# Kernel tuning notes

Measured on AMD Instinct MI355X. Metric: run time of the kernel, lower is better.

Reference implementation:

```python
import jax, jax.numpy as jnp
import numpy as np

ORDER = 4          # signature truncation depth
SCALAR_TERM = True # leading 1 term, as in signatory.signature(..., scalar_term=True)
BATCH, STREAM, CHAN = 2048, 128, 5  # channel = path_dim + 1 (time + 4-dim path)


def _exp_levels(dx, m):
    """Tensor exponential of a single increment dx: levels dx^{(x)k}/k!, k=1..m.
    dx: (B, d). Returns list of (B, d**k) arrays."""
    levels = [dx]
    for k in range(2, m + 1):
        prev = levels[-1]  # (B, d**(k-1))
        levels.append((prev[:, :, None] * dx[:, None, :]).reshape(dx.shape[0], -1) / k)
    return levels


def _chen(S, E):
    """Chen's identity: (S tensor-multiply E) truncated to depth m.
    S, E: tuples/lists of (B, d**k) level arrays (level k at list index k-1)."""
    m = len(E)
    B = E[0].shape[0]
    out = []
    for k in range(m):  # output level k+1
        term = S[k] + E[k]
        for i in range(k):  # S level (i+1) tensor E level (k-i)
            a, b = S[i], E[k - 1 - i]
            term = term + (a[:, :, None] * b[:, None, :]).reshape(B, -1)
        out.append(term)
    return tuple(out)


def _signature(path, m, scalar_term):
    """Truncated path signature, flattened levels 1..m (optionally with leading 1).
    path: (B, T, d) -> (B, [1+] d + d^2 + ... + d^m)."""
    B, T, d = path.shape
    dx = jnp.moveaxis(path[:, 1:] - path[:, :-1], 1, 0)  # (T-1, B, d)
    init = tuple(jnp.zeros((B, d ** k), path.dtype) for k in range(1, m + 1))

    def step(S, inc):
        return _chen(S, _exp_levels(inc, m)), None

    S, _ = jax.lax.scan(step, init, dx)
    sig = jnp.concatenate(S, axis=1)
    if scalar_term:
        sig = jnp.concatenate([jnp.ones((B, 1), path.dtype), sig], axis=1)
    return sig


def setup_inputs() -> dict:
    key = jax.random.key(0)
    kx, ky = jax.random.split(key)
    x = jax.random.normal(kx, (BATCH, STREAM, CHAN), dtype=jnp.float32)
    y = jax.random.normal(ky, (BATCH, STREAM, CHAN), dtype=jnp.float32)
    sigma = jnp.ones((CHAN - 1,), dtype=jnp.float32)  # adversarial scaling params
    return {"x": x, "y": y, "sigma": sigma}


def reference(x, y, sigma):
    # adversarial scaling applied to x's non-time channels only (as in forward())
    mu = jnp.concatenate([x[..., :1], x[..., 1:] * sigma], axis=-1)
    nu = y
    # signatures computed once each and shared across kxx, kxy, kyy (same math)
    sx = _signature(mu, ORDER, SCALAR_TERM)  # (B, P)
    sy = _signature(nu, ORDER, SCALAR_TERM)  # (B, P)
    kxx = jnp.einsum('ip,jp->ij', sx, sx)
    kxy = jnp.einsum('ip,jp->ij', sx, sy)
    kyy = jnp.einsum('ip,jp->ij', sy, sy)
    return jnp.mean(kxx) - 2.0 * jnp.mean(kxy) + jnp.mean(kyy)
```

## Files before the change

### kernel.cpp

```cpp
#include <hip/hip_runtime.h>

typedef float v2f __attribute__((ext_vector_type(2)));

#define BATCH  2048
#define TLEN   128
#define CH     5
#define SIGDIM 780
#define PPB    4
#define NBLK   ((2 * BATCH) / PPB)
#define SEGR   64
#define RBLK   64
#define POISON 0xAAAAAAAAu

__global__ __launch_bounds__(256, 4) void sig_kernel(
    const float* __restrict__ x, const float* __restrict__ y,
    const float* __restrict__ sigma, float* __restrict__ part) {
  const int tid  = threadIdx.x;
  const int wave = tid >> 6;
  const int lane = tid & 63;
  const int h    = lane >> 5;
  const int u    = lane & 31;
  const bool isX = (blockIdx.x < NBLK / 2);
  const int pbase = (isX ? blockIdx.x : blockIdx.x - NBLK / 2) * PPB;
  const int path  = pbase + wave;
  const float* src = (isX ? x : y) + (size_t)path * (TLEN * CH) + h * (SEGR * CH);

  __shared__ __align__(16) float buf[2 * PPB][784];
  __shared__ float blockAcc[SIGDIM];

  for (int i = tid; i < SIGDIM; i += 256) blockAcc[i] = 0.f;

  const float sg0 = sigma[0], sg1 = sigma[1], sg2 = sigma[2], sg3 = sigma[3];

  float* bw = buf[wave * 2 + h];
  if (h == 1 && u < 8) bw[63 * 8 + u] = 0.f;
  const int lim = h ? 63 * CH : 64 * CH;
  for (int i = u; i < lim; i += 32) {
    int t = i / CH, c = i - CH * t;
    float v = src[i + CH] - src[i];
    if (isX && c > 0) {
      const float s = (c == 1) ? sg0 : (c == 2) ? sg1 : (c == 3) ? sg2 : sg3;
      v *= s;
    }
    bw[t * 8 + c] = v;
  }
  __syncthreads();

  const int  uc = u < 25 ? u : 24;
  const int  a_ = uc / 5, b_ = uc - 5 * a_;
  const bool act = (u < 25);

  float s1a = 0.f, s2 = 0.f;
  v2f   s3p0 = {0.f, 0.f}, s3p1 = {0.f, 0.f};
  float s3e = 0.f;
  v2f   s4p0[5] = {{0,0},{0,0},{0,0},{0,0},{0,0}};
  v2f   s4p1[5] = {{0,0},{0,0},{0,0},{0,0},{0,0}};
  float s4e[5]  = {0,0,0,0,0};

  const float* pa_ = bw + a_;
  const float* pb_ = bw + b_;

  for (int g = 0; g < 8; ++g) {
    const float* rg = bw + g * 64;
    const float* ra = pa_ + g * 64;
    const float* rb = pb_ + g * 64;
    #pragma unroll
    for (int k = 0; k < 8; ++k) {
      const float4 m = *(const float4*)(rg + k * 8);
      const float d0 = m.x, d1 = m.y, d2 = m.z, d3 = m.w;
      const float d4 = rg[k * 8 + 4];
      const float da = ra[k * 8];
      const float db = rb[k * 8];
      const float pa = s1a * (1.f / 6.f) + da * (1.f / 24.f);
      const float qa = s1a * 0.5f        + da * (1.f / 6.f);
      const float rr = s1a               + da * 0.5f;
      s1a += da;
      const float p2 = 0.5f * s2 + db * pa;
      const float q2 =        s2 + db * qa;
      s2 += db * rr;
      const v2f dc01 = {d0, d1};
      const v2f dc23 = {d2, d3};
      const v2f p2v  = {p2, p2};
      const v2f q2v  = {q2, q2};
      const v2f p30  = __builtin_elementwise_fma(dc01, p2v, s3p0);
      const v2f p31  = __builtin_elementwise_fma(dc23, p2v, s3p1);
      const float p3e = s3e + d4 * p2;
      s3p0 = __builtin_elementwise_fma(dc01, q2v, s3p0);
      s3p1 = __builtin_elementwise_fma(dc23, q2v, s3p1);
      s3e += d4 * q2;
      #pragma unroll
      for (int d = 0; d < 5; ++d) {
        const float dd = (d == 0) ? d0 : (d == 1) ? d1 : (d == 2) ? d2 : (d == 3) ? d3 : d4;
        const v2f ddv = {dd, dd};
        s4p0[d] = __builtin_elementwise_fma(ddv, p30, s4p0[d]);
        s4p1[d] = __builtin_elementwise_fma(ddv, p31, s4p1[d]);
        s4e[d] += dd * p3e;
      }
    }
  }

  float S3[5] = {s3p0.x, s3p0.y, s3p1.x, s3p1.y, s3e};
  float S4[5][5];
  #pragma unroll
  for (int d = 0; d < 5; ++d) {
    S4[0][d] = s4p0[d].x; S4[1][d] = s4p0[d].y;
    S4[2][d] = s4p1[d].x; S4[3][d] = s4p1[d].y;
    S4[4][d] = s4e[d];
  }

  if (h == 1 && act) {
    float* sgb = bw;
    if (b_ == 0) sgb[a_] = s1a;
    sgb[5 + uc] = s2;
    #pragma unroll
    for (int c = 0; c < 5; ++c) {
      sgb[30 + uc * 5 + c] = S3[c];
      #pragma unroll
      for (int d = 0; d < 5; ++d) sgb[155 + (uc * 5 + c) * 5 + d] = S4[c][d];
    }
  }
  __syncthreads();

  if (h == 0 && act) {
    const float* R = buf[wave * 2 + 1];
    const float o1 = s1a + R[a_];
    const float o2 = s2 + s1a * R[b_] + R[5 + uc];
    if (b_ == 0) atomicAdd(&blockAcc[a_], o1);
    atomicAdd(&blockAcc[5 + uc], o2);
    #pragma unroll
    for (int c = 0; c < 5; ++c) {
      const float o3 = S3[c] + s2 * R[c] + s1a * R[5 + b_ * 5 + c] + R[30 + uc * 5 + c];
      atomicAdd(&blockAcc[30 + uc * 5 + c], o3);
      #pragma unroll
      for (int d = 0; d < 5; ++d) {
        const float o4 = S4[c][d] + S3[c] * R[d] + s2 * R[5 + c * 5 + d]
                       + s1a * R[30 + (b_ * 5 + c) * 5 + d]
                       + R[155 + (uc * 5 + c) * 5 + d];
        atomicAdd(&blockAcc[155 + (uc * 5 + c) * 5 + d], o4);
      }
    }
  }
  __syncthreads();

  const float w = isX ? 1.0f : -1.0f;
  float* pp = part + (size_t)blockIdx.x * SIGDIM;
  for (int i = tid; i < SIGDIM; i += 256) pp[i] = w * blockAcc[i];
}

__global__ __launch_bounds__(256) void red_kernel(
    const float* __restrict__ part, float* __restrict__ acc2,
    unsigned int* __restrict__ counter, float* __restrict__ out) {
  const int tid = threadIdx.x;
  float4 s = {0.f, 0.f, 0.f, 0.f};
  if (tid < SIGDIM / 4) {
    const float* base = part + (size_t)blockIdx.x * (NBLK / RBLK) * SIGDIM + 4 * tid;
    #pragma unroll
    for (int r = 0; r < NBLK / RBLK; ++r) {
      const float4 v = *(const float4*)(base + (size_t)r * SIGDIM);
      s.x += v.x; s.y += v.y; s.z += v.z; s.w += v.w;
    }
    atomicAdd(&acc2[4 * tid + 0], s.x);
    atomicAdd(&acc2[4 * tid + 1], s.y);
    atomicAdd(&acc2[4 * tid + 2], s.z);
    atomicAdd(&acc2[4 * tid + 3], s.w);
  }

  __shared__ float red[4];
  __shared__ unsigned int lastFlag;
  __syncthreads();
  if (tid == 0) {
    __threadfence();
    unsigned int old = __hip_atomic_fetch_add(counter, 1u, __ATOMIC_ACQ_REL,
                                              __HIP_MEMORY_SCOPE_AGENT);
    lastFlag = (old == POISON + (RBLK - 1)) ? 1u : 0u;
  }
  __syncthreads();
  if (lastFlag) {
    float local = 0.f;
    if (tid < SIGDIM / 4) {
      float vx = __hip_atomic_load(&acc2[4 * tid + 0], __ATOMIC_RELAXED, __HIP_MEMORY_SCOPE_AGENT);
      float vy = __hip_atomic_load(&acc2[4 * tid + 1], __ATOMIC_RELAXED, __HIP_MEMORY_SCOPE_AGENT);
      float vz = __hip_atomic_load(&acc2[4 * tid + 2], __ATOMIC_RELAXED, __HIP_MEMORY_SCOPE_AGENT);
      float vw = __hip_atomic_load(&acc2[4 * tid + 3], __ATOMIC_RELAXED, __HIP_MEMORY_SCOPE_AGENT);
      local = vx * vx + vy * vy + vz * vz + vw * vw;
    }
    #pragma unroll
    for (int off = 32; off > 0; off >>= 1) local += __shfl_down(local, off, 64);
    if ((tid & 63) == 0) red[tid >> 6] = local;
    __syncthreads();
    if (tid == 0)
      out[0] = (red[0] + red[1] + red[2] + red[3]) / (2048.0f * 2048.0f);
  }
}

extern "C" void kernel_launch(void* const* d_in, const int* in_sizes, int n_in,
                              void* d_out, int out_size, void* d_ws, size_t ws_size,
                              hipStream_t stream) {
  const float* x     = (const float*)d_in[0];
  const float* y     = (const float*)d_in[1];
  const float* sigma = (const float*)d_in[2];
  float* out = (float*)d_out;
  float* part = (float*)d_ws;
  float* acc2 = (float*)((char*)d_ws + (size_t)NBLK * SIGDIM * sizeof(float));
  unsigned int* counter =
      (unsigned int*)((char*)d_ws + (size_t)NBLK * SIGDIM * sizeof(float)
                      + SIGDIM * sizeof(float));

  sig_kernel<<<dim3(NBLK), dim3(256), 0, stream>>>(x, y, sigma, part);
  red_kernel<<<dim3(RBLK), dim3(256), 0, stream>>>(part, acc2, counter, out);
}
```

Measured before the change: 103.3 us.

## Split each path into four segments and combine with two-level Chen merge

New measurement: 160.4 us. 1.55x slower.

```diff
diff --git a/kernel.cpp b/kernel.cpp
--- a/kernel.cpp
+++ b/kernel.cpp
@@ -6,13 +6,15 @@
 #define TLEN   128
 #define CH     5
 #define SIGDIM 780
-#define PPB    4
-#define NBLK   ((2 * BATCH) / PPB)
-#define SEGR   64
+#define NBLK   2048
+#define NPATH  4096
+#define SEGR   32
+#define SROW   264
 #define RBLK   64
+#define ROWSPB (NPATH / RBLK)
 #define POISON 0xAAAAAAAAu
 
-__global__ __launch_bounds__(256, 4) void sig_kernel(
+__global__ __launch_bounds__(256, 6) void sig_kernel(
     const float* __restrict__ x, const float* __restrict__ y,
     const float* __restrict__ sigma, float* __restrict__ part) {
   const int tid  = threadIdx.x;
@@ -20,21 +22,22 @@
   const int lane = tid & 63;
   const int h    = lane >> 5;
   const int u    = lane & 31;
+  const int q    = wave & 1;
+  const int lp   = wave >> 1;
   const bool isX = (blockIdx.x < NBLK / 2);
-  const int pbase = (isX ? blockIdx.x : blockIdx.x - NBLK / 2) * PPB;
-  const int path  = pbase + wave;
-  const float* src = (isX ? x : y) + (size_t)path * (TLEN * CH) + h * (SEGR * CH);
-
-  __shared__ __align__(16) float buf[2 * PPB][784];
-  __shared__ float blockAcc[SIGDIM];
-
-  for (int i = tid; i < SIGDIM; i += 256) blockAcc[i] = 0.f;
+  const int pbase = (isX ? blockIdx.x : blockIdx.x - NBLK / 2) * 2;
+  const int path  = pbase + lp;
+  const int segIdx = 2 * q + h;
+  const float* src = (isX ? x : y) + (size_t)path * (TLEN * CH) + segIdx * (SEGR * CH);
+
+  __shared__ __align__(16) float segbuf[8][SROW];
+  __shared__ float sigbuf[4][SIGDIM];
 
   const float sg0 = sigma[0], sg1 = sigma[1], sg2 = sigma[2], sg3 = sigma[3];
 
-  float* bw = buf[wave * 2 + h];
-  if (h == 1 && u < 8) bw[63 * 8 + u] = 0.f;
-  const int lim = h ? 63 * CH : 64 * CH;
+  float* bw = segbuf[wave * 2 + h];
+  if (segIdx == 3 && u < 8) bw[31 * 8 + u] = 0.f;
+  const int lim = (segIdx == 3) ? 31 * CH : 32 * CH;
   for (int i = u; i < lim; i += 32) {
     int t = i / CH, c = i - CH * t;
     float v = src[i + CH] - src[i];
@@ -60,7 +63,7 @@
   const float* pa_ = bw + a_;
   const float* pb_ = bw + b_;
 
-  for (int g = 0; g < 8; ++g) {
+  for (int g = 0; g < 4; ++g) {
     const float* rg = bw + g * 64;
     const float* ra = pa_ + g * 64;
     const float* rb = pb_ + g * 64;
@@ -109,7 +112,7 @@
   }
 
   if (h == 1 && act) {
-    float* sgb = bw;
+    float* sgb = sigbuf[wave];
     if (b_ == 0) sgb[a_] = s1a;
     sgb[5 + uc] = s2;
     #pragma unroll
@@ -121,41 +124,77 @@
   }
   __syncthreads();
 
+  float o1 = 0.f, o2 = 0.f, o3[5], o4[5][5];
   if (h == 0 && act) {
-    const float* R = buf[wave * 2 + 1];
-    const float o1 = s1a + R[a_];
-    const float o2 = s2 + s1a * R[b_] + R[5 + uc];
-    if (b_ == 0) atomicAdd(&blockAcc[a_], o1);
-    atomicAdd(&blockAcc[5 + uc], o2);
-    #pragma unroll
-    for (int c = 0; c < 5; ++c) {
-      const float o3 = S3[c] + s2 * R[c] + s1a * R[5 + b_ * 5 + c] + R[30 + uc * 5 + c];
-      atomicAdd(&blockAcc[30 + uc * 5 + c], o3);
-      #pragma unroll
-      for (int d = 0; d < 5; ++d) {
-        const float o4 = S4[c][d] + S3[c] * R[d] + s2 * R[5 + c * 5 + d]
-                       + s1a * R[30 + (b_ * 5 + c) * 5 + d]
-                       + R[155 + (uc * 5 + c) * 5 + d];
-        atomicAdd(&blockAcc[155 + (uc * 5 + c) * 5 + d], o4);
-      }
+    const float* R = sigbuf[wave];
+    o1 = s1a + R[a_];
+    o2 = s2 + s1a * R[b_] + R[5 + uc];
+    #pragma unroll
+    for (int c = 0; c < 5; ++c) {
+      o3[c] = S3[c] + s2 * R[c] + s1a * R[5 + b_ * 5 + c] + R[30 + uc * 5 + c];
+      #pragma unroll
+      for (int d = 0; d < 5; ++d)
+        o4[c][d] = S4[c][d] + S3[c] * R[d] + s2 * R[5 + c * 5 + d]
+                 + s1a * R[30 + (b_ * 5 + c) * 5 + d]
+                 + R[155 + (uc * 5 + c) * 5 + d];
+    }
+  }
+  if (q == 1 && h == 0 && act) {
+    float* sgb = sigbuf[wave];
+    if (b_ == 0) sgb[a_] = o1;
+    sgb[5 + uc] = o2;
+    #pragma unroll
+    for (int c = 0; c < 5; ++c) {
+      sgb[30 + uc * 5 + c] = o3[c];
+      #pragma unroll
+      for (int d = 0; d < 5; ++d) sgb[155 + (uc * 5 + c) * 5 + d] = o4[c][d];
+    }
+  }
+  __syncthreads();
+
+  if (q == 0 && h == 0 && act) {
+    const float* R = sigbuf[wave + 1];
+    float f1 = o1 + R[a_];
+    float f2 = o2 + o1 * R[b_] + R[5 + uc];
+    float f3[5], f4[5][5];
+    #pragma unroll
+    for (int c = 0; c < 5; ++c) {
+      f3[c] = o3[c] + o2 * R[c] + o1 * R[5 + b_ * 5 + c] + R[30 + uc * 5 + c];
+      #pragma unroll
+      for (int d = 0; d < 5; ++d)
+        f4[c][d] = o4[c][d] + o3[c] * R[d] + o2 * R[5 + c * 5 + d]
+                 + o1 * R[30 + (b_ * 5 + c) * 5 + d]
+                 + R[155 + (uc * 5 + c) * 5 + d];
+    }
+    float* sgb = sigbuf[wave];
+    if (b_ == 0) sgb[a_] = f1;
+    sgb[5 + uc] = f2;
+    #pragma unroll
+    for (int c = 0; c < 5; ++c) {
+      sgb[30 + uc * 5 + c] = f3[c];
+      #pragma unroll
+      for (int d = 0; d < 5; ++d) sgb[155 + (uc * 5 + c) * 5 + d] = f4[c][d];
     }
   }
   __syncthreads();
 
   const float w = isX ? 1.0f : -1.0f;
-  float* pp = part + (size_t)blockIdx.x * SIGDIM;
-  for (int i = tid; i < SIGDIM; i += 256) pp[i] = w * blockAcc[i];
+  for (int i = tid; i < 2 * SIGDIM; i += 256) {
+    const int p = (i < SIGDIM) ? 0 : 1;
+    const int j = i - p * SIGDIM;
+    part[(size_t)(blockIdx.x * 2 + p) * SIGDIM + j] = w * sigbuf[2 * p][j];
+  }
 }
 
 __global__ __launch_bounds__(256) void red_kernel(
     const float* __restrict__ part, float* __restrict__ acc2,
     unsigned int* __restrict__ counter, float* __restrict__ out) {
   const int tid = threadIdx.x;
-  float4 s = {0.f, 0.f, 0.f, 0.f};
   if (tid < SIGDIM / 4) {
-    const float* base = part + (size_t)blockIdx.x * (NBLK / RBLK) * SIGDIM + 4 * tid;
-    #pragma unroll
-    for (int r = 0; r < NBLK / RBLK; ++r) {
+    float4 s = {0.f, 0.f, 0.f, 0.f};
+    const float* base = part + (size_t)blockIdx.x * ROWSPB * SIGDIM + 4 * tid;
+    #pragma unroll 8
+    for (int r = 0; r < ROWSPB; ++r) {
       const float4 v = *(const float4*)(base + (size_t)r * SIGDIM);
       s.x += v.x; s.y += v.y; s.z += v.z; s.w += v.w;
     }
@@ -201,9 +240,9 @@
   const float* sigma = (const float*)d_in[2];
   float* out = (float*)d_out;
   float* part = (float*)d_ws;
-  float* acc2 = (float*)((char*)d_ws + (size_t)NBLK * SIGDIM * sizeof(float));
+  float* acc2 = (float*)((char*)d_ws + (size_t)NPATH * SIGDIM * sizeof(float));
   unsigned int* counter =
-      (unsigned int*)((char*)d_ws + (size_t)NBLK * SIGDIM * sizeof(float)
+      (unsigned int*)((char*)d_ws + (size_t)NPATH * SIGDIM * sizeof(float)
                       + SIGDIM * sizeof(float));
 
   sig_kernel<<<dim3(NBLK), dim3(256), 0, stream>>>(x, y, sigma, part);
```
